# Kernel tuning notes

Hardware: AMD Instinct MI355X
Metric: run time of the kernel (lower is better)

## Reference

```python
import jax, jax.numpy as jnp
import numpy as np

B, S, D, E, K = 4, 2048, 2048, 64, 2

def setup_inputs() -> dict:
    key = jax.random.key(0)
    k1, k2, k3, k4 = jax.random.split(key, 4)
    x = jax.random.normal(k1, (B, S, D), dtype=jnp.float32)
    W = jax.random.normal(k2, (E, D), dtype=jnp.float32) * 0.02  # gate_linear.weight
    noise_weight = jax.random.normal(k3, (E,), dtype=jnp.float32) * 0.02
    noise = jax.random.normal(k4, (B, S, E), dtype=jnp.float32)  # torch.randn_like(logits), noisy_std=1.0
    return {"x": x, "W": W, "noise_weight": noise_weight, "noise": noise, "k": K}

def reference(x, W, noise_weight, noise, k):
    # logits = x @ W.T  -> [B, S, E]
    logits = jnp.einsum('bsd,ed->bse', x, W)
    # noise injection: randn * noisy_std(=1.0) * noise_weight (per-expert scale)
    logits_noisy = logits + noise * noise_weight
    # top-k over experts
    top_vals, top_idx = jax.lax.top_k(logits_noisy, k)  # [B, S, k]
    # softmax over a tensor that is -inf everywhere except the top-k slots is
    # exactly: zeros everywhere, softmax(top_vals) scattered into the top-k slots.
    probs = jax.nn.softmax(top_vals, axis=-1)  # [B, S, k]
    n_tok = B * S
    rows = jnp.arange(n_tok)[:, None]  # [n_tok, 1]
    gated = jnp.zeros((n_tok, E), dtype=logits.dtype)
    gated = gated.at[rows, top_idx.reshape(n_tok, k)].set(probs.reshape(n_tok, k))
    gated = gated.reshape(B, S, E)
    return gated, top_idx, top_vals
```

## Files before the change

kernel.cpp:

```cpp
#include <hip/hip_runtime.h>
#include <math.h>

#define NTOK 8192
#define DDIM 2048
#define NEXP 64
#define MT   16
#define ASTR 72
#define CSTR 68

#define GATED_SZ (NTOK * NEXP)
#define IDX_OFF  GATED_SZ
#define VALS_OFF (GATED_SZ + NTOK * 2)

#define NKSTEP (DDIM / 32)
#define NTILE  (NEXP / 16)
#define BFRAG_HALVES ((size_t)NKSTEP * NTILE * 64 * 8)

typedef _Float16 f16x8 __attribute__((ext_vector_type(8)));
typedef _Float16 f16x4 __attribute__((ext_vector_type(4)));
typedef float    f32x4 __attribute__((ext_vector_type(4)));

__global__ void pack_b_kernel(const float* __restrict__ W,
                              _Float16* __restrict__ Bh,
                              _Float16* __restrict__ Bl)
{
    const int tid  = blockIdx.x * blockDim.x + threadIdx.x;
    const int lane = tid & 63;
    const int fid  = tid >> 6;
    const int ks   = fid >> 2;
    const int nt   = fid & 3;
    const int e    = nt * 16 + (lane & 15);
    const int k    = ks * 32 + (lane >> 4) * 8;
    const float* src = W + (size_t)e * DDIM + k;

    f16x8 hi, lo;
#pragma unroll
    for (int j = 0; j < 8; ++j) {
        const float v = src[j];
        const _Float16 h = (_Float16)v;
        hi[j] = h;
        lo[j] = (_Float16)((v - (float)h) * 4096.f);
    }
    *(f16x8*)(Bh + (size_t)tid * 8) = hi;
    *(f16x8*)(Bl + (size_t)tid * 8) = lo;
}

#define BFRAG(base, ks, nt) \
    (*(const f16x8*)((base) + ((((size_t)(ks)) * 4 + (nt)) * 64 + lane) * 8))

static __device__ __forceinline__ void cvt_hilo4(float4 v, f16x4& h4, f16x4& l4)
{
    const float vv[4] = {v.x, v.y, v.z, v.w};
#pragma unroll
    for (int j = 0; j < 4; ++j) {
        const _Float16 hh = (_Float16)vv[j];
        h4[j] = hh;
        l4[j] = (_Float16)((vv[j] - (float)hh) * 4096.f);
    }
}

__global__ __launch_bounds__(512, 2) void gate_kernel(
    const float* __restrict__ x,
    const _Float16* __restrict__ Bh,
    const _Float16* __restrict__ Bl,
    const float* __restrict__ noise_w,
    const float* __restrict__ noise,
    float* __restrict__ out)
{
    __shared__ __align__(16) char smem_raw[8 * 2 * MT * ASTR * 2];

    const int tid  = threadIdx.x;
    const int lane = tid & 63;
    const int w    = __builtin_amdgcn_readfirstlane(tid >> 6);
    const int tokBase = blockIdx.x * MT;

    const int q = lane >> 4;
    const int m = lane & 15;

    _Float16* xs = (_Float16*)smem_raw + (size_t)w * (2 * MT * ASTR);

    const float* xw = x + (size_t)tokBase * DDIM + (size_t)w * 256;

    float4 xr[4][4];
#pragma unroll
    for (int s = 0; s < 4; ++s)
#pragma unroll
        for (int p = 0; p < 4; ++p)
            xr[s][p] = *(const float4*)(xw + (size_t)(p * 4 + q) * DDIM
                                        + s * 64 + m * 4);

    const float nwv = noise_w[lane];
    const float nz0 = noise[(size_t)(tokBase + w * 2)     * NEXP + lane];
    const float nz1 = noise[(size_t)(tokBase + w * 2 + 1) * NEXP + lane];

    f32x4 acc_hh[4], acc_lo[4];
#pragma unroll
    for (int nt = 0; nt < 4; ++nt) {
        acc_hh[nt] = (f32x4){0.f, 0.f, 0.f, 0.f};
        acc_lo[nt] = (f32x4){0.f, 0.f, 0.f, 0.f};
    }

#pragma unroll
    for (int s = 0; s < 4; ++s) {
#pragma unroll
        for (int p = 0; p < 4; ++p) {
            f16x4 h4, l4;
            cvt_hilo4(xr[s][p], h4, l4);
            const int off = (p * 4 + q) * ASTR + m * 4;
            *(f16x4*)&xs[off] = h4;
            *(f16x4*)&xs[MT * ASTR + off] = l4;
        }
#pragma unroll
        for (int stp = 0; stp < 2; ++stp) {
            const int ks = w * 8 + s * 2 + stp;
            const f16x8 ah = *(const f16x8*)&xs[m * ASTR + stp * 32 + q * 8];
            const f16x8 al = *(const f16x8*)&xs[MT * ASTR + m * ASTR + stp * 32 + q * 8];
#pragma unroll
            for (int nt = 0; nt < 4; ++nt) {
                const f16x8 bh = BFRAG(Bh, ks, nt);
                const f16x8 bl = BFRAG(Bl, ks, nt);
                acc_hh[nt] = __builtin_amdgcn_mfma_f32_16x16x32_f16(ah, bh, acc_hh[nt], 0, 0, 0);
                acc_lo[nt] = __builtin_amdgcn_mfma_f32_16x16x32_f16(ah, bl, acc_lo[nt], 0, 0, 0);
                acc_lo[nt] = __builtin_amdgcn_mfma_f32_16x16x32_f16(al, bh, acc_lo[nt], 0, 0, 0);
            }
        }
    }

    __syncthreads();
    float* cbuf = (float*)smem_raw;

#pragma unroll
    for (int nt = 0; nt < 4; ++nt) {
        const int e = nt * 16 + m;
#pragma unroll
        for (int r = 0; r < 4; ++r) {
            const int t = q * 4 + r;
            cbuf[((w * MT) + t) * CSTR + e] =
                acc_hh[nt][r] + acc_lo[nt][r] * (1.f / 4096.f);
        }
    }
    __syncthreads();

#pragma unroll
    for (int i = 0; i < 2; ++i) {
        const int t   = w * 2 + i;
        const int tok = tokBase + t;
        const int e   = lane;

        float v = 0.f;
#pragma unroll
        for (int p = 0; p < 8; ++p)
            v += cbuf[((p * MT) + t) * CSTR + e];
        v += (i ? nz1 : nz0) * nwv;

        float m1 = v; int i1 = e;
#pragma unroll
        for (int sh = 32; sh > 0; sh >>= 1) {
            float ov = __shfl_xor(m1, sh, 64);
            int   oi = __shfl_xor(i1, sh, 64);
            if (ov > m1 || (ov == m1 && oi < i1)) { m1 = ov; i1 = oi; }
        }
        float vm = (e == i1) ? -INFINITY : v;
        float m2 = vm; int i2 = e;
#pragma unroll
        for (int sh = 32; sh > 0; sh >>= 1) {
            float ov = __shfl_xor(m2, sh, 64);
            int   oi = __shfl_xor(i2, sh, 64);
            if (ov > m2 || (ov == m2 && oi < i2)) { m2 = ov; i2 = oi; }
        }

        const float e2  = expf(m2 - m1);
        const float inv = 1.f / (1.f + e2);
        const float p1  = inv;
        const float p2  = e2 * inv;

        float gval = 0.f;
        if (e == i1) gval = p1;
        else if (e == i2) gval = p2;
        out[(size_t)tok * NEXP + e] = gval;

        if (lane == 0) {
            out[IDX_OFF  + tok * 2 + 0] = (float)i1;
            out[IDX_OFF  + tok * 2 + 1] = (float)i2;
            out[VALS_OFF + tok * 2 + 0] = m1;
            out[VALS_OFF + tok * 2 + 1] = m2;
        }
    }
}

extern "C" void kernel_launch(void* const* d_in, const int* in_sizes, int n_in,
                              void* d_out, int out_size, void* d_ws, size_t ws_size,
                              hipStream_t stream) {
    const float* x     = (const float*)d_in[0];
    const float* W     = (const float*)d_in[1];
    const float* nw    = (const float*)d_in[2];
    const float* noise = (const float*)d_in[3];
    float* out = (float*)d_out;

    _Float16* Bh = (_Float16*)d_ws;
    _Float16* Bl = Bh + BFRAG_HALVES;

    hipLaunchKernelGGL(pack_b_kernel, dim3(64), dim3(256), 0, stream, W, Bh, Bl);

    hipLaunchKernelGGL(gate_kernel, dim3(NTOK / MT), dim3(512), 0, stream,
                       x, Bh, Bl, nw, noise, out);
}
```

Before: 112.5 us.

## Load x directly as MFMA B-operand and swap operand roles, drop LDS staging

```diff
diff --git a/kernel.cpp b/kernel.cpp
--- a/kernel.cpp
+++ b/kernel.cpp
@@ -5,7 +5,7 @@
 #define DDIM 2048
 #define NEXP 64
 #define MT   16
-#define ASTR 72
+#define NW   8
 #define CSTR 68
 
 #define GATED_SZ (NTOK * NEXP)
@@ -17,7 +17,6 @@
 #define BFRAG_HALVES ((size_t)NKSTEP * NTILE * 64 * 8)
 
 typedef _Float16 f16x8 __attribute__((ext_vector_type(8)));
-typedef _Float16 f16x4 __attribute__((ext_vector_type(4)));
 typedef float    f32x4 __attribute__((ext_vector_type(4)));
 
 __global__ void pack_b_kernel(const float* __restrict__ W,
@@ -45,17 +44,18 @@
     *(f16x8*)(Bl + (size_t)tid * 8) = lo;
 }
 
-#define BFRAG(base, ks, nt) \
-    (*(const f16x8*)((base) + ((((size_t)(ks)) * 4 + (nt)) * 64 + lane) * 8))
-
-static __device__ __forceinline__ void cvt_hilo4(float4 v, f16x4& h4, f16x4& l4)
+#define BFRAG(base, ks, et) \
+    (*(const f16x8*)((base) + ((((size_t)(ks)) * 4 + (et)) * 64 + lane) * 8))
+
+static __device__ __forceinline__ void cvt_hilo8(float4 v0, float4 v1,
+                                                 f16x8& h8, f16x8& l8)
 {
-    const float vv[4] = {v.x, v.y, v.z, v.w};
-#pragma unroll
-    for (int j = 0; j < 4; ++j) {
+    const float vv[8] = {v0.x, v0.y, v0.z, v0.w, v1.x, v1.y, v1.z, v1.w};
+#pragma unroll
+    for (int j = 0; j < 8; ++j) {
         const _Float16 hh = (_Float16)vv[j];
-        h4[j] = hh;
-        l4[j] = (_Float16)((vv[j] - (float)hh) * 4096.f);
+        h8[j] = hh;
+        l8[j] = (_Float16)((vv[j] - (float)hh) * 4096.f);
     }
 }
 
@@ -67,7 +67,7 @@
     const float* __restrict__ noise,
     float* __restrict__ out)
 {
-    __shared__ __align__(16) char smem_raw[8 * 2 * MT * ASTR * 2];
+    __shared__ float cbuf[NW * MT * CSTR];
 
     const int tid  = threadIdx.x;
     const int lane = tid & 63;
@@ -77,17 +77,7 @@
     const int q = lane >> 4;
     const int m = lane & 15;
 
-    _Float16* xs = (_Float16*)smem_raw + (size_t)w * (2 * MT * ASTR);
-
-    const float* xw = x + (size_t)tokBase * DDIM + (size_t)w * 256;
-
-    float4 xr[4][4];
-#pragma unroll
-    for (int s = 0; s < 4; ++s)
-#pragma unroll
-        for (int p = 0; p < 4; ++p)
-            xr[s][p] = *(const float4*)(xw + (size_t)(p * 4 + q) * DDIM
-                                        + s * 64 + m * 4);
+    const float* xp = x + (size_t)(tokBase + m) * DDIM + w * 256 + q * 8;
 
     const float nwv = noise_w[lane];
     const float nz0 = noise[(size_t)(tokBase + w * 2)     * NEXP + lane];
@@ -95,49 +85,55 @@
 
     f32x4 acc_hh[4], acc_lo[4];
 #pragma unroll
-    for (int nt = 0; nt < 4; ++nt) {
-        acc_hh[nt] = (f32x4){0.f, 0.f, 0.f, 0.f};
-        acc_lo[nt] = (f32x4){0.f, 0.f, 0.f, 0.f};
-    }
-
-#pragma unroll
-    for (int s = 0; s < 4; ++s) {
-#pragma unroll
-        for (int p = 0; p < 4; ++p) {
-            f16x4 h4, l4;
-            cvt_hilo4(xr[s][p], h4, l4);
-            const int off = (p * 4 + q) * ASTR + m * 4;
-            *(f16x4*)&xs[off] = h4;
-            *(f16x4*)&xs[MT * ASTR + off] = l4;
-        }
-#pragma unroll
-        for (int stp = 0; stp < 2; ++stp) {
-            const int ks = w * 8 + s * 2 + stp;
-            const f16x8 ah = *(const f16x8*)&xs[m * ASTR + stp * 32 + q * 8];
-            const f16x8 al = *(const f16x8*)&xs[MT * ASTR + m * ASTR + stp * 32 + q * 8];
-#pragma unroll
-            for (int nt = 0; nt < 4; ++nt) {
-                const f16x8 bh = BFRAG(Bh, ks, nt);
-                const f16x8 bl = BFRAG(Bl, ks, nt);
-                acc_hh[nt] = __builtin_amdgcn_mfma_f32_16x16x32_f16(ah, bh, acc_hh[nt], 0, 0, 0);
-                acc_lo[nt] = __builtin_amdgcn_mfma_f32_16x16x32_f16(ah, bl, acc_lo[nt], 0, 0, 0);
-                acc_lo[nt] = __builtin_amdgcn_mfma_f32_16x16x32_f16(al, bh, acc_lo[nt], 0, 0, 0);
-            }
-        }
-    }
-
-    __syncthreads();
-    float* cbuf = (float*)smem_raw;
-
-#pragma unroll
-    for (int nt = 0; nt < 4; ++nt) {
-        const int e = nt * 16 + m;
-#pragma unroll
-        for (int r = 0; r < 4; ++r) {
-            const int t = q * 4 + r;
-            cbuf[((w * MT) + t) * CSTR + e] =
-                acc_hh[nt][r] + acc_lo[nt][r] * (1.f / 4096.f);
-        }
+    for (int et = 0; et < 4; ++et) {
+        acc_hh[et] = (f32x4){0.f, 0.f, 0.f, 0.f};
+        acc_lo[et] = (f32x4){0.f, 0.f, 0.f, 0.f};
+    }
+
+#define XLOAD(buf, s)                                                        \
+    {                                                                        \
+        buf[0] = *(const float4*)(xp + (s) * 32);                            \
+        buf[1] = *(const float4*)(xp + (s) * 32 + 4);                        \
+    }
+
+#define STEP(s, buf)                                                         \
+    {                                                                        \
+        f16x8 xh_, xl_;                                                      \
+        cvt_hilo8(buf[0], buf[1], xh_, xl_);                                 \
+        if ((s) + 2 < 8) XLOAD(buf, (s) + 2)       \
+        const int ks = w * 8 + (s);                                          \
+        _Pragma("unroll")                                                    \
+        for (int et = 0; et < 4; ++et) {                                     \
+            const f16x8 wh_ = BFRAG(Bh, ks, et);                             \
+            const f16x8 wl_ = BFRAG(Bl, ks, et);                             \
+            acc_hh[et] = __builtin_amdgcn_mfma_f32_16x16x32_f16(wh_, xh_, acc_hh[et], 0, 0, 0); \
+            acc_lo[et] = __builtin_amdgcn_mfma_f32_16x16x32_f16(wh_, xl_, acc_lo[et], 0, 0, 0); \
+            acc_lo[et] = __builtin_amdgcn_mfma_f32_16x16x32_f16(wl_, xh_, acc_lo[et], 0, 0, 0); \
+        }                                                                    \
+    }
+
+    float4 bufA[2], bufB[2];
+    XLOAD(bufA, 0)
+    XLOAD(bufB, 1)
+    STEP(0, bufA)
+    STEP(1, bufB)
+    STEP(2, bufA)
+    STEP(3, bufB)
+    STEP(4, bufA)
+    STEP(5, bufB)
+    STEP(6, bufA)
+    STEP(7, bufB)
+
+#undef XLOAD
+#undef STEP
+
+#pragma unroll
+    for (int et = 0; et < 4; ++et) {
+        f32x4 cv;
+#pragma unroll
+        for (int r = 0; r < 4; ++r)
+            cv[r] = acc_hh[et][r] + acc_lo[et][r] * (1.f / 4096.f);
+        *(f32x4*)&cbuf[((size_t)w * MT + m) * CSTR + et * 16 + q * 4] = cv;
     }
     __syncthreads();
 
@@ -150,7 +146,7 @@
         float v = 0.f;
 #pragma unroll
         for (int p = 0; p < 8; ++p)
-            v += cbuf[((p * MT) + t) * CSTR + e];
+            v += cbuf[((size_t)p * MT + t) * CSTR + e];
         v += (i ? nz1 : nz0) * nwv;
 
         float m1 = v; int i1 = e;
```

After: 118.3 us. 1.05x slower.
